# Optimization experiments

Measured on AMD Instinct MI355X. Metric: run time of the kernel, lower is better.

Reference implementation:

```python
import jax, jax.numpy as jnp
import numpy as np

N_NODES = 50000
EPS = 1e-5


def _gcn_edges(edge_index, num_nodes):
    # Add self loops (PyG GCNConv default) and compute symmetric normalization.
    src = jnp.concatenate([edge_index[0], jnp.arange(num_nodes, dtype=edge_index.dtype)])
    dst = jnp.concatenate([edge_index[1], jnp.arange(num_nodes, dtype=edge_index.dtype)])
    deg = jax.ops.segment_sum(jnp.ones_like(dst, dtype=jnp.float32), dst, num_segments=num_nodes)
    dinv = jnp.where(deg > 0, jax.lax.rsqrt(deg), 0.0)
    norm = dinv[src] * dinv[dst]  # [E+N]
    return src, dst, norm


def gcn_conv(x, W, b, src, dst, norm, num_nodes):
    xw = x @ W  # [N, out]
    msg = xw[src] * norm[:, None]  # [E+N, out] gather + scale
    out = jax.ops.segment_sum(msg, dst, num_segments=num_nodes)  # scatter-add
    return out + b


def layer_norm(x, g, b):
    mu = jnp.mean(x, axis=-1, keepdims=True)
    var = jnp.mean(jnp.square(x - mu), axis=-1, keepdims=True)
    return (x - mu) * jax.lax.rsqrt(var + EPS) * g + b


def setup_inputs() -> dict:
    key = jax.random.key(0)
    ks = jax.random.split(key, 12)
    d_in, d_h, d_out = 128, 128, 64
    n_edges = 800000
    x = jax.random.normal(ks[0], (N_NODES, d_in), dtype=jnp.float32)
    edge_index = jax.random.randint(ks[1], (2, n_edges), 0, N_NODES, dtype=jnp.int64)
    s = 1.0 / np.sqrt(d_in)
    return {
        "x": x,
        "edge_index": edge_index,
        "W1": jax.random.uniform(ks[2], (d_in, d_h), jnp.float32, -s, s),
        "b1": jnp.zeros((d_h,), jnp.float32),
        "W2": jax.random.uniform(ks[3], (d_h, d_h), jnp.float32, -s, s),
        "b2": jnp.zeros((d_h,), jnp.float32),
        "W3": jax.random.uniform(ks[4], (d_h, d_out), jnp.float32, -s, s),
        "b3": jnp.zeros((d_out,), jnp.float32),
        "g1": jnp.ones((d_h,), jnp.float32),
        "be1": jnp.zeros((d_h,), jnp.float32),
        "g2": jnp.ones((d_h,), jnp.float32),
        "be2": jnp.zeros((d_h,), jnp.float32),
    }


def reference(x, edge_index, W1, b1, W2, b2, W3, b3, g1, be1, g2, be2):
    num_nodes = x.shape[0]
    src, dst, norm = _gcn_edges(edge_index, num_nodes)
    h = jax.nn.relu(gcn_conv(x, W1, b1, src, dst, norm, num_nodes))
    h = layer_norm(h, g1, be1)  # dropout is identity in eval mode
    h = jax.nn.relu(gcn_conv(h, W2, b2, src, dst, norm, num_nodes))
    h = layer_norm(h, g2, be2)
    return gcn_conv(h, W3, b3, src, dst, norm, num_nodes)
```

## Files before the change

kernel.cpp:

```cpp
#include <hip/hip_runtime.h>

#define EPSV 1e-5f

typedef _Float16 half2_t __attribute__((ext_vector_type(2)));
typedef _Float16 half8_t __attribute__((ext_vector_type(8)));
typedef float float4_t __attribute__((ext_vector_type(4)));

#define BINSH 6
#define BINSZ 64


__global__ __launch_bounds__(256) void k_init(
    const float* __restrict__ W1, const float* __restrict__ W2,
    const float* __restrict__ W3, _Float16* __restrict__ Wh1,
    _Float16* __restrict__ Wh2, _Float16* __restrict__ Wh3,
    const int* __restrict__ src, const int* __restrict__ dst,
    int* __restrict__ cursor, int* __restrict__ csr, int E, int N) {
  int bid = blockIdx.x;
  if (bid < 20) {
    const float* W;
    _Float16* Wh;
    int COLS, t;
    if (bid < 8) { W = W1; Wh = Wh1; COLS = 128; t = bid * 256 + threadIdx.x; }
    else if (bid < 16) { W = W2; Wh = Wh2; COLS = 128; t = (bid - 8) * 256 + threadIdx.x; }
    else { W = W3; Wh = Wh3; COLS = 64; t = (bid - 16) * 256 + threadIdx.x; }
    int NT = (COLS / 16) * 4 * 64;
    if (t >= NT) return;
    int lane = t & 63;
    int ks = (t >> 6) & 3;
    int nb = t >> 8;
    int col = nb * 16 + (lane & 15);
    int k0 = ks * 32 + (lane >> 4) * 8;
    half8_t v;
#pragma unroll
    for (int j = 0; j < 8; j++) v[j] = (_Float16)W[(size_t)(k0 + j) * COLS + col];
    *(half8_t*)&Wh[(size_t)t * 8] = v;
    return;
  }
  int b = bid - 20;
  int slice = b & 7;
  int lo = (int)(((long long)N * slice) >> 3);
  int hi = (int)(((long long)N * (slice + 1)) >> 3);
  int r = (b >> 3) * 256 + threadIdx.x;
  int stride = (4096 >> 3) * 256;
  for (int e = r; e < E; e += stride) {
    int d = __builtin_nontemporal_load(&dst[e]);
    if (d >= lo && d < hi) {
      int s = __builtin_nontemporal_load(&src[e]);
      int pos = atomicAdd(&cursor[d], 1);
      if (pos < BINSZ) csr[((size_t)d << BINSH) + pos] = s;
    }
  }
}


template <int COLS, bool LN, typename AT>
__device__ __forceinline__ void gemm_body(
    int bx, const AT* __restrict__ A, const float2* __restrict__ lnp,
    const float* __restrict__ g, const float* __restrict__ be,
    const _Float16* __restrict__ Wh, const int* __restrict__ cursor,
    _Float16* __restrict__ out, int N, int N1) {
  constexpr int NB = COLS / 16;
  int lane = threadIdx.x & 63;
  int w = threadIdx.x >> 6;
  int quad = lane >> 4;
  int mrow = bx * 64 + w * 16 + (lane & 15);
  half8_t af[4];
  if (mrow < N) {
    if constexpr (LN) {
      float P = 0.f, Q = 0.f;
#pragma unroll
      for (int s = 0; s < 4; s++) {
        float2 pq = lnp[(size_t)s * N + mrow];
        P += pq.x; Q += pq.y;
      }
      float mean = P * (1.f / 128.f);
      float rstd = rsqrtf(Q * (1.f / 128.f) - mean * mean + EPSV);
#pragma unroll
      for (int ks = 0; ks < 4; ks++) {
        half8_t sv = *(const half8_t*)&A[((size_t)ks * N1 + mrow) * 32 + quad * 8];
        float4 g0 = *(const float4*)&g[ks * 32 + quad * 8];
        float4 g1 = *(const float4*)&g[ks * 32 + quad * 8 + 4];
        float4 e0 = *(const float4*)&be[ks * 32 + quad * 8];
        float4 e1 = *(const float4*)&be[ks * 32 + quad * 8 + 4];
        af[ks][0] = (_Float16)fmaf(((float)sv[0] - mean) * rstd, g0.x, e0.x);
        af[ks][1] = (_Float16)fmaf(((float)sv[1] - mean) * rstd, g0.y, e0.y);
        af[ks][2] = (_Float16)fmaf(((float)sv[2] - mean) * rstd, g0.z, e0.z);
        af[ks][3] = (_Float16)fmaf(((float)sv[3] - mean) * rstd, g0.w, e0.w);
        af[ks][4] = (_Float16)fmaf(((float)sv[4] - mean) * rstd, g1.x, e1.x);
        af[ks][5] = (_Float16)fmaf(((float)sv[5] - mean) * rstd, g1.y, e1.y);
        af[ks][6] = (_Float16)fmaf(((float)sv[6] - mean) * rstd, g1.z, e1.z);
        af[ks][7] = (_Float16)fmaf(((float)sv[7] - mean) * rstd, g1.w, e1.w);
      }
    } else {
      const AT* ap = A + (size_t)mrow * 128 + quad * 8;
#pragma unroll
      for (int ks = 0; ks < 4; ks++) {
        float4 f0 = *(const float4*)(ap + ks * 32);
        float4 f1 = *(const float4*)(ap + ks * 32 + 4);
        af[ks][0] = (_Float16)f0.x; af[ks][1] = (_Float16)f0.y;
        af[ks][2] = (_Float16)f0.z; af[ks][3] = (_Float16)f0.w;
        af[ks][4] = (_Float16)f1.x; af[ks][5] = (_Float16)f1.y;
        af[ks][6] = (_Float16)f1.z; af[ks][7] = (_Float16)f1.w;
      }
    }
  } else {
#pragma unroll
    for (int ks = 0; ks < 4; ks++)
#pragma unroll
      for (int j = 0; j < 8; j++) af[ks][j] = (_Float16)0.f;
  }
  float4_t acc[NB];
#pragma unroll
  for (int nb = 0; nb < NB; nb++) acc[nb] = (float4_t){0.f, 0.f, 0.f, 0.f};
#pragma unroll
  for (int nb = 0; nb < NB; nb++) {
#pragma unroll
    for (int ks = 0; ks < 4; ks++) {
      half8_t bf = *(const half8_t*)&Wh[(size_t)((nb * 4 + ks) * 64 + lane) * 8];
      acc[nb] = __builtin_amdgcn_mfma_f32_16x16x32_f16(af[ks], bf, acc[nb], 0, 0, 0);
    }
  }
  int orow0 = bx * 64 + w * 16 + quad * 4;
#pragma unroll
  for (int r = 0; r < 4; r++) {
    int row = orow0 + r;
    if (row < N) {
      float dv = rsqrtf((float)(min(cursor[row], BINSZ) + 1));
#pragma unroll
      for (int nb = 0; nb < NB; nb++) {
        int dim = nb * 16 + (lane & 15);
        out[((size_t)(dim >> 5) * N1 + row) * 32 + (dim & 31)] =
            (_Float16)(acc[nb][r] * dv);
      }
    }
  }
}


__global__ __launch_bounds__(256) void k_gemm1_prep(
    const float* __restrict__ x, const _Float16* __restrict__ Wh1,
    const int* __restrict__ cursor, int* __restrict__ csr,
    _Float16* __restrict__ ys_y, _Float16* __restrict__ ys3,
    int N, int N1, int gb) {
  if ((int)blockIdx.x < gb) {
    gemm_body<128, false, float>(blockIdx.x, x, nullptr, nullptr, nullptr, Wh1,
                                 cursor, ys_y, N, N1);
    return;
  }
  int i = (blockIdx.x - gb) * 256 + threadIdx.x;
  if (i < N) {
    int cnt = min(cursor[i], BINSZ);
    int cr = (cnt + 15) & ~15;
    for (int p = cnt; p < cr; p++) csr[((size_t)i << BINSH) + p] = N;
  }
  if (i < 64) {
    ((half2_t*)ys_y)[((size_t)(i >> 4) * N1 + N) * 16 + (i & 15)] = (half2_t){0, 0};
  } else if (i < 96) {
    int j = i - 64;
    ((half2_t*)ys3)[((size_t)(j >> 4) * N1 + N) * 16 + (j & 15)] = (half2_t){0, 0};
  }
}

template <int COLS, bool LN, typename AT>
__global__ __launch_bounds__(256) void k_gemm_mfma(
    const AT* __restrict__ A, const float2* __restrict__ lnp,
    const float* __restrict__ g, const float* __restrict__ be,
    const _Float16* __restrict__ Wh, const int* __restrict__ cursor,
    _Float16* __restrict__ out, int N, int N1) {
  gemm_body<COLS, LN, AT>(blockIdx.x, A, lnp, g, be, Wh, cursor, out, N, N1);
}


__global__ __launch_bounds__(256) void k_aggs(
    const _Float16* __restrict__ ysrc, const int* __restrict__ csr,
    const int* __restrict__ cursor, const float* __restrict__ b,
    _Float16* __restrict__ sdst, float2* __restrict__ lnp, int N, int N1) {
  int slice = blockIdx.x & 3;
  int lane = threadIdx.x & 63;
  int g = lane >> 4, li = lane & 15;
  int node = (blockIdx.x >> 2) * 16 + (threadIdx.x >> 6) * 4 + g;
  const half2_t* yb = (const half2_t*)ysrc + (size_t)slice * N1 * 16;
  int cnt = 0;
  if (node < N) cnt = min(cursor[node], BINSZ);
  int cround = (cnt + 15) & ~15;
  size_t bin = (size_t)node << BINSH;
  float a0 = 0.f, a1 = 0.f;
  for (int c = 0; c < cround; c += 16) {
    int idx = csr[bin + c + li];
#pragma unroll
    for (int e = 0; e < 16; e++) {
      int s = __shfl(idx, (g << 4) | e, 64);
      half2_t u = yb[(size_t)s * 16 + li];
      a0 += (float)u[0];
      a1 += (float)u[1];
    }
  }
  half2_t us = yb[(size_t)min(node, N) * 16 + li];
  a0 += (float)us[0];
  a1 += (float)us[1];
  float di = rsqrtf((float)(cnt + 1));
  float2 bb = ((const float2*)b)[slice * 16 + li];
  float v0 = fmaxf(fmaf(a0, di, bb.x), 0.f);
  float v1 = fmaxf(fmaf(a1, di, bb.y), 0.f);
  float p = v0 + v1, q = fmaf(v0, v0, v1 * v1);
#pragma unroll
  for (int o = 1; o < 16; o <<= 1) {
    p += __shfl_xor(p, o, 64);
    q += __shfl_xor(q, o, 64);
  }
  if (node < N) {
    if (li == 0) lnp[(size_t)slice * N + node] = make_float2(p, q);
    half2_t o2;
    o2[0] = (_Float16)v0;
    o2[1] = (_Float16)v1;
    ((half2_t*)sdst)[((size_t)slice * N1 + node) * 16 + li] = o2;
  }
}


__global__ __launch_bounds__(256) void k_agg_out(
    const _Float16* __restrict__ ysrc, const int* __restrict__ csr,
    const int* __restrict__ cursor, const float* __restrict__ b,
    float* __restrict__ out, int N, int N1) {
  int slice = blockIdx.x & 1;
  int lane = threadIdx.x & 63;
  int g = lane >> 4, li = lane & 15;
  int node = (blockIdx.x >> 1) * 16 + (threadIdx.x >> 6) * 4 + g;
  const half2_t* yb = (const half2_t*)ysrc + (size_t)slice * N1 * 16;
  int cnt = 0;
  if (node < N) cnt = min(cursor[node], BINSZ);
  int cround = (cnt + 15) & ~15;
  size_t bin = (size_t)node << BINSH;
  float a0 = 0.f, a1 = 0.f;
  for (int c = 0; c < cround; c += 16) {
    int idx = csr[bin + c + li];
#pragma unroll
    for (int e = 0; e < 16; e++) {
      int s = __shfl(idx, (g << 4) | e, 64);
      half2_t u = yb[(size_t)s * 16 + li];
      a0 += (float)u[0];
      a1 += (float)u[1];
    }
  }
  if (node < N) {
    half2_t us = yb[(size_t)node * 16 + li];
    a0 += (float)us[0];
    a1 += (float)us[1];
    float di = rsqrtf((float)(cnt + 1));
    float2 bb = ((const float2*)b)[slice * 16 + li];
    float2 o;
    o.x = fmaf(a0, di, bb.x);
    o.y = fmaf(a1, di, bb.y);
    ((float2*)out)[(size_t)node * 32 + slice * 16 + li] = o;
  }
}


extern "C" void kernel_launch(void* const* d_in, const int* in_sizes, int n_in,
                              void* d_out, int out_size, void* d_ws, size_t ws_size,
                              hipStream_t stream) {
  const float* x = (const float*)d_in[0];
  const int* ei = (const int*)d_in[1];
  const float* W1 = (const float*)d_in[2];
  const float* b1 = (const float*)d_in[3];
  const float* W2 = (const float*)d_in[4];
  const float* b2 = (const float*)d_in[5];
  const float* W3 = (const float*)d_in[6];
  const float* b3 = (const float*)d_in[7];
  const float* g1 = (const float*)d_in[8];
  const float* be1 = (const float*)d_in[9];
  const float* g2 = (const float*)d_in[10];
  const float* be2 = (const float*)d_in[11];

  int N = in_sizes[0] / 128;
  int E = in_sizes[1] / 2;
  int N1 = N + 1;
  const int* srcs = ei;
  const int* dsts = ei + E;

  char* ws = (char*)d_ws;
  size_t off = 0;
  auto alloc = [&](size_t bytes) -> char* {
    char* p = ws + off;
    off = (off + bytes + 255) & ~(size_t)255;
    return p;
  };
  int* cursor = (int*)alloc((size_t)N * 4);
  int* csr = (int*)alloc((size_t)N * BINSZ * 4);
  _Float16* ys_y = (_Float16*)alloc((size_t)4 * N1 * 32 * 2);
  _Float16* ys_s = (_Float16*)alloc((size_t)4 * N1 * 32 * 2);
  _Float16* ys3 = (_Float16*)alloc((size_t)2 * N1 * 32 * 2);
  float2* lnp = (float2*)alloc((size_t)4 * N * 8);
  _Float16* Wh1 = (_Float16*)alloc(128 * 128 * 2);
  _Float16* Wh2 = (_Float16*)alloc(128 * 128 * 2);
  _Float16* Wh3 = (_Float16*)alloc(128 * 64 * 2);

  int gb = (N + 63) / 64;
  int pb = (N + 255) / 256;
  int nb16 = (N + 15) / 16;

  hipMemsetAsync(cursor, 0, (size_t)N * sizeof(int), stream);
  k_init<<<4116, 256, 0, stream>>>(W1, W2, W3, Wh1, Wh2, Wh3,
                                   srcs, dsts, cursor, csr, E, N);
  k_gemm1_prep<<<gb + pb, 256, 0, stream>>>(x, Wh1, cursor, csr, ys_y, ys3,
                                            N, N1, gb);
  k_aggs<<<nb16 * 4, 256, 0, stream>>>(ys_y, csr, cursor, b1, ys_s, lnp, N, N1);
  k_gemm_mfma<128, true, _Float16><<<gb, 256, 0, stream>>>(
      ys_s, lnp, g1, be1, Wh2, cursor, ys_y, N, N1);
  k_aggs<<<nb16 * 4, 256, 0, stream>>>(ys_y, csr, cursor, b2, ys_s, lnp, N, N1);
  k_gemm_mfma<64, true, _Float16><<<gb, 256, 0, stream>>>(
      ys_s, lnp, g2, be2, Wh3, cursor, ys3, N, N1);
  k_agg_out<<<nb16 * 2, 256, 0, stream>>>(ys3, csr, cursor, b3,
                                          (float*)d_out, N, N1);
}
```

Measured before the change: 260.8 us.

## Widen aggregation gathers to 16-byte loads with edge-split lanes and fdot2 accumulation

In both aggregation kernels each lane now loads a half8 (16 bytes) per neighbor instead of a half2. The 16 lanes of a node split into 4 feature quarters times 4 edge subsets, and partial sums are combined with cross-lane xor shuffles at the end. Accumulation uses perm plus fdot2 against ones so packed fp16 pairs are added in fewer instructions. The aim is fewer, wider memory transactions and fewer shuffles per edge, at the cost of extra reduction shuffles and more accumulator registers.

```diff
diff --git a/kernel.cpp b/kernel.cpp
--- a/kernel.cpp
+++ b/kernel.cpp
@@ -179,42 +179,76 @@
   int slice = blockIdx.x & 3;
   int lane = threadIdx.x & 63;
   int g = lane >> 4, li = lane & 15;
+  int q = li & 3, es = li >> 2;
   int node = (blockIdx.x >> 2) * 16 + (threadIdx.x >> 6) * 4 + g;
-  const half2_t* yb = (const half2_t*)ysrc + (size_t)slice * N1 * 16;
+  const half8_t* yb = (const half8_t*)ysrc + (size_t)slice * N1 * 4;
   int cnt = 0;
   if (node < N) cnt = min(cursor[node], BINSZ);
   int cround = (cnt + 15) & ~15;
   size_t bin = (size_t)node << BINSH;
-  float a0 = 0.f, a1 = 0.f;
+  float acc[8];
+#pragma unroll
+  for (int j = 0; j < 8; j++) acc[j] = 0.f;
+  const half2_t one2 = {(_Float16)1.f, (_Float16)1.f};
   for (int c = 0; c < cround; c += 16) {
     int idx = csr[bin + c + li];
 #pragma unroll
-    for (int e = 0; e < 16; e++) {
-      int s = __shfl(idx, (g << 4) | e, 64);
-      half2_t u = yb[(size_t)s * 16 + li];
-      a0 += (float)u[0];
-      a1 += (float)u[1];
-    }
-  }
-  half2_t us = yb[(size_t)min(node, N) * 16 + li];
-  a0 += (float)us[0];
-  a1 += (float)us[1];
+    for (int p = 0; p < 2; p++) {
+      int sa = __shfl(idx, (g << 4) | (es << 2) | (p << 1), 64);
+      int sb = __shfl(idx, (g << 4) | (es << 2) | (p << 1) | 1, 64);
+      half8_t ua = yb[(size_t)sa * 4 + q];
+      half8_t ub = yb[(size_t)sb * 4 + q];
+      const unsigned int* wa = (const unsigned int*)&ua;
+      const unsigned int* wb = (const unsigned int*)&ub;
+#pragma unroll
+      for (int w = 0; w < 4; w++) {
+        unsigned int p0 = __builtin_amdgcn_perm(wa[w], wb[w], 0x01000504u);
+        unsigned int p1 = __builtin_amdgcn_perm(wa[w], wb[w], 0x03020706u);
+        acc[2 * w] = __builtin_amdgcn_fdot2(
+            __builtin_bit_cast(half2_t, p0), one2, acc[2 * w], false);
+        acc[2 * w + 1] = __builtin_amdgcn_fdot2(
+            __builtin_bit_cast(half2_t, p1), one2, acc[2 * w + 1], false);
+      }
+    }
+  }
+#pragma unroll
+  for (int j = 0; j < 8; j++) {
+    acc[j] += __shfl_xor(acc[j], 4, 64);
+    acc[j] += __shfl_xor(acc[j], 8, 64);
+  }
+  half8_t us = yb[(size_t)min(node, N) * 4 + q];
+#pragma unroll
+  for (int j = 0; j < 8; j++) acc[j] += (float)us[j];
   float di = rsqrtf((float)(cnt + 1));
-  float2 bb = ((const float2*)b)[slice * 16 + li];
-  float v0 = fmaxf(fmaf(a0, di, bb.x), 0.f);
-  float v1 = fmaxf(fmaf(a1, di, bb.y), 0.f);
-  float p = v0 + v1, q = fmaf(v0, v0, v1 * v1);
-#pragma unroll
-  for (int o = 1; o < 16; o <<= 1) {
-    p += __shfl_xor(p, o, 64);
-    q += __shfl_xor(q, o, 64);
-  }
+  float4 b0 = ((const float4*)b)[slice * 8 + q * 2];
+  float4 b1 = ((const float4*)b)[slice * 8 + q * 2 + 1];
+  float v[8];
+  v[0] = fmaxf(fmaf(acc[0], di, b0.x), 0.f);
+  v[1] = fmaxf(fmaf(acc[1], di, b0.y), 0.f);
+  v[2] = fmaxf(fmaf(acc[2], di, b0.z), 0.f);
+  v[3] = fmaxf(fmaf(acc[3], di, b0.w), 0.f);
+  v[4] = fmaxf(fmaf(acc[4], di, b1.x), 0.f);
+  v[5] = fmaxf(fmaf(acc[5], di, b1.y), 0.f);
+  v[6] = fmaxf(fmaf(acc[6], di, b1.z), 0.f);
+  v[7] = fmaxf(fmaf(acc[7], di, b1.w), 0.f);
+  float p = 0.f, qs = 0.f;
+#pragma unroll
+  for (int j = 0; j < 8; j++) {
+    p += v[j];
+    qs = fmaf(v[j], v[j], qs);
+  }
+  p += __shfl_xor(p, 1, 64);
+  p += __shfl_xor(p, 2, 64);
+  qs += __shfl_xor(qs, 1, 64);
+  qs += __shfl_xor(qs, 2, 64);
   if (node < N) {
-    if (li == 0) lnp[(size_t)slice * N + node] = make_float2(p, q);
-    half2_t o2;
-    o2[0] = (_Float16)v0;
-    o2[1] = (_Float16)v1;
-    ((half2_t*)sdst)[((size_t)slice * N1 + node) * 16 + li] = o2;
+    if (li == 0) lnp[(size_t)slice * N + node] = make_float2(p, qs);
+    if (es == 0) {
+      half8_t o;
+#pragma unroll
+      for (int j = 0; j < 8; j++) o[j] = (_Float16)v[j];
+      ((half8_t*)sdst)[((size_t)slice * N1 + node) * 4 + q] = o;
+    }
   }
 }
 
@@ -226,33 +260,61 @@
   int slice = blockIdx.x & 1;
   int lane = threadIdx.x & 63;
   int g = lane >> 4, li = lane & 15;
+  int q = li & 3, es = li >> 2;
   int node = (blockIdx.x >> 1) * 16 + (threadIdx.x >> 6) * 4 + g;
-  const half2_t* yb = (const half2_t*)ysrc + (size_t)slice * N1 * 16;
+  const half8_t* yb = (const half8_t*)ysrc + (size_t)slice * N1 * 4;
   int cnt = 0;
   if (node < N) cnt = min(cursor[node], BINSZ);
   int cround = (cnt + 15) & ~15;
   size_t bin = (size_t)node << BINSH;
-  float a0 = 0.f, a1 = 0.f;
+  float acc[8];
+#pragma unroll
+  for (int j = 0; j < 8; j++) acc[j] = 0.f;
+  const half2_t one2 = {(_Float16)1.f, (_Float16)1.f};
   for (int c = 0; c < cround; c += 16) {
     int idx = csr[bin + c + li];
 #pragma unroll
-    for (int e = 0; e < 16; e++) {
-      int s = __shfl(idx, (g << 4) | e, 64);
-      half2_t u = yb[(size_t)s * 16 + li];
-      a0 += (float)u[0];
-      a1 += (float)u[1];
-    }
-  }
-  if (node < N) {
-    half2_t us = yb[(size_t)node * 16 + li];
-    a0 += (float)us[0];
-    a1 += (float)us[1];
+    for (int p = 0; p < 2; p++) {
+      int sa = __shfl(idx, (g << 4) | (es << 2) | (p << 1), 64);
+      int sb = __shfl(idx, (g << 4) | (es << 2) | (p << 1) | 1, 64);
+      half8_t ua = yb[(size_t)sa * 4 + q];
+      half8_t ub = yb[(size_t)sb * 4 + q];
+      const unsigned int* wa = (const unsigned int*)&ua;
+      const unsigned int* wb = (const unsigned int*)&ub;
+#pragma unroll
+      for (int w = 0; w < 4; w++) {
+        unsigned int p0 = __builtin_amdgcn_perm(wa[w], wb[w], 0x01000504u);
+        unsigned int p1 = __builtin_amdgcn_perm(wa[w], wb[w], 0x03020706u);
+        acc[2 * w] = __builtin_amdgcn_fdot2(
+            __builtin_bit_cast(half2_t, p0), one2, acc[2 * w], false);
+        acc[2 * w + 1] = __builtin_amdgcn_fdot2(
+            __builtin_bit_cast(half2_t, p1), one2, acc[2 * w + 1], false);
+      }
+    }
+  }
+#pragma unroll
+  for (int j = 0; j < 8; j++) {
+    acc[j] += __shfl_xor(acc[j], 4, 64);
+    acc[j] += __shfl_xor(acc[j], 8, 64);
+  }
+  if (node < N && es == 0) {
+    half8_t us = yb[(size_t)node * 4 + q];
+#pragma unroll
+    for (int j = 0; j < 8; j++) acc[j] += (float)us[j];
     float di = rsqrtf((float)(cnt + 1));
-    float2 bb = ((const float2*)b)[slice * 16 + li];
-    float2 o;
-    o.x = fmaf(a0, di, bb.x);
-    o.y = fmaf(a1, di, bb.y);
-    ((float2*)out)[(size_t)node * 32 + slice * 16 + li] = o;
+    float4 b0 = ((const float4*)b)[slice * 8 + q * 2];
+    float4 b1 = ((const float4*)b)[slice * 8 + q * 2 + 1];
+    float4 o0, o1;
+    o0.x = fmaf(acc[0], di, b0.x);
+    o0.y = fmaf(acc[1], di, b0.y);
+    o0.z = fmaf(acc[2], di, b0.z);
+    o0.w = fmaf(acc[3], di, b0.w);
+    o1.x = fmaf(acc[4], di, b1.x);
+    o1.y = fmaf(acc[5], di, b1.y);
+    o1.z = fmaf(acc[6], di, b1.z);
+    o1.w = fmaf(acc[7], di, b1.w);
+    ((float4*)out)[(size_t)node * 16 + slice * 8 + q * 2] = o0;
+    ((float4*)out)[(size_t)node * 16 + slice * 8 + q * 2 + 1] = o1;
   }
 }
 
```

Result: faster. 245.3 us (-5.9%).
